# Optimization experiments

Measured on AMD Instinct MI355X. Metric: run time of the kernel, lower is better.

## Reference

```python
import jax, jax.numpy as jnp
import numpy as np
from math import sqrt

N_HEADS = 16

def setup_inputs() -> dict:
    key = jax.random.key(0)
    ks = jax.random.split(key, 6)
    B, T, C = 4, 2048, 1024
    s = 0.02
    return {
        "X": jax.random.normal(ks[0], (B, T, C), jnp.float32),
        "Wq": jax.random.normal(ks[1], (C, C), jnp.float32) * s,
        "Wk": jax.random.normal(ks[2], (C, C), jnp.float32) * s,
        "Wv": jax.random.normal(ks[3], (C, C), jnp.float32) * s,
        "Wo": jax.random.normal(ks[4], (C, C), jnp.float32) * s,
        "bo": jnp.zeros((C,), jnp.float32),
    }

def reference(X, Wq, Wk, Wv, Wo, bo):
    B, T, C = X.shape
    H = N_HEADS
    D = C // H
    scale = sqrt(C / H)  # == sqrt(D)
    # Linear layers (torch Linear: y = x @ W.T), split into heads: [B,H,T,D]
    Q = (X @ Wq.T).reshape(B, T, H, D).transpose(0, 2, 1, 3)
    K = (X @ Wk.T).reshape(B, T, H, D).transpose(0, 2, 1, 3)
    V = (X @ Wv.T).reshape(B, T, H, D).transpose(0, 2, 1, 3)
    A = jnp.einsum("bhtd,bhsd->bhts", Q, K) / scale  # [B,H,T,T]
    causal = jnp.tril(jnp.ones((T, T), dtype=bool))
    A = jnp.where(causal, A, -jnp.inf)
    A = jax.nn.softmax(A, axis=-1)
    Y = jnp.einsum("bhts,bhsd->bhtd", A, V)  # [B,H,T,D]
    Y = Y.transpose(0, 2, 1, 3).reshape(B, T, C)
    return Y @ Wo.T + bo
```

## Files before the change

### kernel.cpp

```cpp
#include <hip/hip_runtime.h>
#include <hip/hip_bf16.h>
#include <stdint.h>


typedef unsigned short u16;
typedef __attribute__((ext_vector_type(8))) __bf16 bf16x8;
typedef __attribute__((ext_vector_type(4))) float  f32x4;
typedef __attribute__((ext_vector_type(4))) unsigned short u16x4;
typedef __attribute__((ext_vector_type(8))) unsigned short u16x8;
typedef __attribute__((ext_vector_type(4))) short s16x4;

#define B_  4
#define T_  2048
#define C_  1024
#define H_  16
#define D_  64
#define BT_ (B_ * T_)
#define NT_ 16

#define Q_SCALE 0.1803368801111204f

__device__ __forceinline__ u16 f32_to_bf16(float f) {
    unsigned int u = __float_as_uint(f);
    unsigned int r = (u + 0x7FFFu + ((u >> 16) & 1u)) >> 16;
    return (u16)r;
}

__device__ __forceinline__ unsigned int pk_bf16(float a, float b) {
    float2 f2; f2.x = a; f2.y = b;
    __hip_bfloat162 h = __float22bfloat162_rn(f2);
    return *(unsigned int*)&h;
}

__device__ __forceinline__ void async16(const void* g, void* lds) {
    __builtin_amdgcn_global_load_lds(
        (const __attribute__((address_space(1))) void*)g,
        (__attribute__((address_space(3))) void*)lds, 16, 0, 0);
}

__global__ void cast_all_kernel(const float* __restrict__ X,
                                const float* __restrict__ w0, const float* __restrict__ w1,
                                const float* __restrict__ w2, const float* __restrict__ w3,
                                u16* __restrict__ xo,
                                u16* __restrict__ o0, u16* __restrict__ o1,
                                u16* __restrict__ o2, u16* __restrict__ o3) {
    int id = blockIdx.x;
    const float* in; u16* out; int i;
    if (id < 8192) {
        in = X; out = xo; i = id * 256 + threadIdx.x;
    } else {
        int k = (id - 8192) >> 10;
        in  = (k == 0) ? w0 : (k == 1) ? w1 : (k == 2) ? w2 : w3;
        out = (k == 0) ? o0 : (k == 1) ? o1 : (k == 2) ? o2 : o3;
        i = ((id - 8192) & 1023) * 256 + threadIdx.x;
    }
    float4 v = ((const float4*)in)[i];
    u16x4 o;
    o[0] = f32_to_bf16(v.x); o[1] = f32_to_bf16(v.y);
    o[2] = f32_to_bf16(v.z); o[3] = f32_to_bf16(v.w);
    ((u16x4*)out)[i] = o;
}

#define PH384(CB, P, ISSUE, GATE)                                              \
  {                                                                            \
    if ((P) == 0) {                                                            \
      _Pragma("unroll") for (int mi = 0; mi < 4; ++mi)                         \
        _Pragma("unroll") for (int ks = 0; ks < 2; ++ks)                       \
          xf[mi][ks] = *(const bf16x8*)((CB) + axoff[mi][ks]);                 \
    }                                                                          \
    _Pragma("unroll") for (int e = 0; e < 2; ++e)                              \
      _Pragma("unroll") for (int ks = 0; ks < 2; ++ks)                         \
        wf[e][ks] = *(const bf16x8*)((CB) + bwoff[2 * (P) + e][ks]);           \
    ISSUE;                                                                     \
    if ((P) == 0) asm volatile("s_waitcnt lgkmcnt(8)" ::: "memory");           \
    if ((GATE) == 6) asm volatile("s_waitcnt vmcnt(6)" ::: "memory");          \
    else if ((GATE) == 0) asm volatile("s_waitcnt vmcnt(0)" ::: "memory");     \
    __builtin_amdgcn_s_barrier();                                              \
    asm volatile("" ::: "memory");                                             \
    __builtin_amdgcn_s_setprio(1);                                             \
    _Pragma("unroll") for (int mi = 0; mi < 4; ++mi)                           \
      _Pragma("unroll") for (int e = 0; e < 2; ++e) {                          \
        f32x4 a_ = acc[mi][2 * (P) + e];                                       \
        if (SWAPV) {                                                           \
          a_ = __builtin_amdgcn_mfma_f32_16x16x32_bf16(xf[mi][0], wf[e][0], a_, 0, 0, 0); \
          a_ = __builtin_amdgcn_mfma_f32_16x16x32_bf16(xf[mi][1], wf[e][1], a_, 0, 0, 0); \
        } else {                                                               \
          a_ = __builtin_amdgcn_mfma_f32_16x16x32_bf16(wf[e][0], xf[mi][0], a_, 0, 0, 0); \
          a_ = __builtin_amdgcn_mfma_f32_16x16x32_bf16(wf[e][1], xf[mi][1], a_, 0, 0, 0); \
        }                                                                      \
        acc[mi][2 * (P) + e] = a_;                                             \
      }                                                                        \
    __builtin_amdgcn_s_setprio(0);                                             \
    asm volatile("" ::: "memory");                                             \
    __builtin_amdgcn_s_barrier();                                              \
    asm volatile("" ::: "memory");                                             \
  }

template<bool SWAPV>
__device__ __forceinline__ void qkv384_core(const u16* __restrict__ Arow,
                                            const u16* __restrict__ Brow,
                                            char* lds, f32x4 (&acc)[4][6])
{
    int tid = threadIdx.x, lane = tid & 63, w = tid >> 6;
    int quad = lane >> 4, l15 = lane & 15;
    int wm = w >> 2, wn = w & 3;

    int gc = (((tid & 7) - (tid >> 3)) & 7) * 8;
    const u16* asrc = Arow + (size_t)(tid >> 3) * C_ + gc;
    const u16* bsrc = Brow + (size_t)(tid >> 3) * C_ + gc;

    auto issue_unit = [&](int kt, int u) {
        char* d = lds + ((kt & 1) << 16) + (u << 14) + (w << 10);
        int ko = kt * 64;
        const u16* s = (u == 0) ? (asrc + ko)
                                : (bsrc + (size_t)(u - 1) * 128 * C_ + ko);
        async16(s, d);
        async16(s + (size_t)64 * C_, d + 8192);
    };

    int axoff[4][2], bwoff[6][2];
#pragma unroll
    for (int mi = 0; mi < 4; ++mi) {
        int r = wm * 64 + mi * 16 + l15;
#pragma unroll
        for (int ks = 0; ks < 2; ++ks)
            axoff[mi][ks] = r * 128 + (((ks * 4 + quad + r) & 7) << 4);
    }
#pragma unroll
    for (int nj = 0; nj < 6; ++nj) {
        int r = wn * 32 + (nj & 1) * 16 + l15;
#pragma unroll
        for (int ks = 0; ks < 2; ++ks)
            bwoff[nj][ks] = (1 + (nj >> 1)) * 16384 + r * 128 + (((ks * 4 + quad + r) & 7) << 4);
    }

    bf16x8 xf[4][2];
    bf16x8 wf[2][2];

    issue_unit(0, 0); issue_unit(0, 1); issue_unit(0, 2); issue_unit(0, 3);
    issue_unit(1, 0); issue_unit(1, 1); issue_unit(1, 2);
    asm volatile("s_waitcnt vmcnt(6)" ::: "memory");
    __builtin_amdgcn_s_barrier();
    asm volatile("" ::: "memory");

    for (int t = 0; t < NT_; ++t) {
        char* cb = lds + ((t & 1) << 16);
        PH384(cb, 0, { if (t + 1 < NT_) issue_unit(t + 1, 3); }, -1);
        PH384(cb, 1, { if (t + 2 < NT_) { issue_unit(t + 2, 0); issue_unit(t + 2, 1); } }, -1);
        int gate = (t < NT_ - 2) ? 6 : ((t == NT_ - 2) ? 0 : -1);
        PH384(cb, 2, { if (t + 2 < NT_) issue_unit(t + 2, 2); }, gate);
    }
}

__global__ __launch_bounds__(512, 2) void qkv_gemm384(
    const u16* __restrict__ Xb, const u16* __restrict__ Wcat,
    u16* __restrict__ Qb, u16* __restrict__ Kb, u16* __restrict__ Vtb)
{
    __shared__ __attribute__((aligned(128))) char LDSRAW[131072];

    int id = blockIdx.x;
    int wg = (id & 7) * 64 + (id >> 3);
    int bn = wg >> 6;
    int bm = wg & 63;
    int m0 = bm * 128;
    int chb = bn * 384;

    const u16* Arow = Xb   + (size_t)m0  * C_;
    const u16* Brow = Wcat + (size_t)chb * C_;

    f32x4 acc[4][6];
    const f32x4 z4 = {0.f, 0.f, 0.f, 0.f};
#pragma unroll
    for (int i = 0; i < 4; ++i)
#pragma unroll
        for (int j = 0; j < 6; ++j) acc[i][j] = z4;

    int tid = threadIdx.x, lane = tid & 63, w = tid >> 6;
    int quad = lane >> 4, l15 = lane & 15;
    int wm = w >> 2, wn = w & 3;

    if (bn < 6) {
        qkv384_core<false>(Arow, Brow, LDSRAW, acc);
#pragma unroll
        for (int mi = 0; mi < 4; ++mi) {
            int tg = m0 + wm * 64 + mi * 16 + l15;
#pragma unroll
            for (int nj = 0; nj < 6; ++nj) {
                int colb = chb + (nj >> 1) * 128 + wn * 32 + (nj & 1) * 16 + quad * 4;
                if (colb < 2048) {
                    u16* OUT = (colb < 1024) ? Qb : Kb;
                    float sc = (colb < 1024) ? Q_SCALE : 1.0f;
                    u16x4 v;
#pragma unroll
                    for (int rr = 0; rr < 4; ++rr) v[rr] = f32_to_bf16(acc[mi][nj][rr] * sc);
                    *(u16x4*)&OUT[(size_t)tg * C_ + (colb & 1023)] = v;
                } else {
                    int b_ = tg >> 11, tl = tg & (T_ - 1);
#pragma unroll
                    for (int rr = 0; rr < 4; ++rr) {
                        int ch = colb + rr;
                        int h = (ch >> 6) & 15, d = ch & 63;
                        Vtb[((size_t)(b_ * H_ + h) * D_ + d) * T_ + tl] =
                            f32_to_bf16(acc[mi][nj][rr]);
                    }
                }
            }
        }
    } else {
        qkv384_core<true>(Arow, Brow, LDSRAW, acc);
#pragma unroll
        for (int mi = 0; mi < 4; ++mi) {
            int t0 = m0 + wm * 64 + mi * 16 + quad * 4;
            int b_ = t0 >> 11, tl = t0 & (T_ - 1);
#pragma unroll
            for (int nj = 0; nj < 6; ++nj) {
                int ch = chb + (nj >> 1) * 128 + wn * 32 + (nj & 1) * 16 + l15;
                int h = (ch >> 6) & 15, d = ch & 63;
                u16x4 v;
#pragma unroll
                for (int rr = 0; rr < 4; ++rr) v[rr] = f32_to_bf16(acc[mi][nj][rr]);
                *(u16x4*)&Vtb[((size_t)(b_ * H_ + h) * D_ + d) * T_ + tl] = v;
            }
        }
    }
}

template<bool SWAP>
__device__ __forceinline__ void gemm8_core(const u16* __restrict__ Arow,
                                           const u16* __restrict__ Brow,
                                           char* lds, f32x4 (&acc)[4][4])
{
    int tid  = threadIdx.x;
    int lane = tid & 63, w = tid >> 6;
    int quad = lane >> 4, l15 = lane & 15;
    int wm = w >> 2, wn = w & 3;

    int r  = tid >> 2, s4 = tid & 3;
    int kg = ((s4 - (r >> 1)) & 3) * 8;
    const u16* xsrc  = Arow + (size_t)r * C_ + kg;
    const u16* wsrc0 = Brow + (size_t)r * C_ + kg;
    const u16* wsrc1 = Brow + (size_t)(128 + r) * C_ + kg;
    int wu = w << 10;

    int xoff[4], woff[4];
#pragma unroll
    for (int i = 0; i < 4; ++i) {
        int rx = wm * 64 + i * 16 + l15;
        xoff[i] = rx * 64 + (((rx >> 1) + quad) & 3) * 16;
        int rw = wn * 64 + i * 16 + l15;
        woff[i] = 16384 + rw * 64 + (((rw >> 1) + quad) & 3) * 16;
    }

    auto issue_group = [&](int g) {
        int db = (g >> 1) & 1, ks = g & 1;
        int koff = (g >> 1) * 64 + ks * 32;
        char* ldb = lds + db * 49152;
        async16(xsrc  + koff, ldb + ks * 8192 + wu);
        async16(wsrc0 + koff, ldb + 16384 + ks * 16384 + wu);
        async16(wsrc1 + koff, ldb + 16384 + ks * 16384 + 8192 + wu);
    };

    issue_group(0); issue_group(1); issue_group(2);
    asm volatile("s_waitcnt vmcnt(6)" ::: "memory");
    __builtin_amdgcn_s_barrier();
    asm volatile("" ::: "memory");

    for (int t = 0; t < NT_; ++t) {
        char* cb = lds + (t & 1) * 49152;
#pragma unroll
        for (int p = 0; p < 2; ++p) {
            bf16x8 xf[4], wf[4];
            const char* xb = cb + p * 8192;
            const char* wb = cb + p * 16384;
#pragma unroll
            for (int i = 0; i < 4; ++i) xf[i] = *(const bf16x8*)(xb + xoff[i]);
#pragma unroll
            for (int j = 0; j < 4; ++j) wf[j] = *(const bf16x8*)(wb + woff[j]);

            int g = 2 * t + 3 + p;
            if (g < 2 * NT_) issue_group(g);

            if (t < NT_ - 2) {
                asm volatile("s_waitcnt vmcnt(6)" ::: "memory");
            } else if (t == NT_ - 2) {
                if (p == 0) asm volatile("s_waitcnt vmcnt(6)" ::: "memory");
                else        asm volatile("s_waitcnt vmcnt(3)" ::: "memory");
            } else {
                if (p == 0) asm volatile("s_waitcnt vmcnt(0)" ::: "memory");
            }
            asm volatile("" ::: "memory");
            __builtin_amdgcn_s_barrier();
            asm volatile("" ::: "memory");

            __builtin_amdgcn_s_setprio(1);
#pragma unroll
            for (int i = 0; i < 4; ++i)
#pragma unroll
                for (int j = 0; j < 4; ++j) {
                    if (SWAP)
                        acc[i][j] = __builtin_amdgcn_mfma_f32_16x16x32_bf16(xf[i], wf[j], acc[i][j], 0, 0, 0);
                    else
                        acc[i][j] = __builtin_amdgcn_mfma_f32_16x16x32_bf16(wf[j], xf[i], acc[i][j], 0, 0, 0);
                }
            __builtin_amdgcn_s_setprio(0);
            asm volatile("" ::: "memory");
            __builtin_amdgcn_s_barrier();
            asm volatile("" ::: "memory");
        }
    }
}

__global__ __launch_bounds__(256, 4) void attn_kernel(
    const u16* __restrict__ Qb, const u16* __restrict__ Kb,
    const u16* __restrict__ Vtb, u16* __restrict__ Yb)
{
    __shared__ u16 SMA[16384];
    u16* Ks0 = SMA;
    u16* Ks1 = SMA + 4096;
    u16* Vs0 = SMA + 8192;
    u16* Vs1 = SMA + 12288;

    int id = blockIdx.x;
    int bh = id & 63;
    int jj = id >> 6;

    int tid = threadIdx.x, lane = tid & 63, w = tid >> 6;
    int quad = lane >> 4, l15 = lane & 15;
    int b = bh >> 4, h = bh & 15;

    int koff0[4], koff1[4], voff[4][4];
#pragma unroll
    for (int sblk = 0; sblk < 4; ++sblk) {
        int sr = sblk * 16 + l15;
        koff0[sblk] = (sr * 64 + ((quad + sr) & 7) * 8) * 2;
        koff1[sblk] = (sr * 64 + ((4 + quad + sr) & 7) * 8) * 2;
    }
#pragma unroll
    for (int n = 0; n < 4; ++n)
#pragma unroll
        for (int sblk = 0; sblk < 4; ++sblk) {
            int dr = n * 16 + l15;
            voff[n][sblk] = (dr * 64 + ((sblk * 2 + (quad >> 1) + dr) & 7) * 8 + (quad & 1) * 4) * 2;
        }

    int cA = tid, cB = tid + 256;
    int sA = cA >> 3, sB = cB >> 3;
    int offA = (((cA & 7) - sA) & 7) * 8;
    int offB = (((cB & 7) - sB) & 7) * 8;
    const u16* Kbase = Kb + (size_t)(b * T_) * C_ + h * 64;
    const u16* Vbase = Vtb + (size_t)bh * D_ * T_;
    int ldsb0 = (w * 64) * 16, ldsb1 = (256 + w * 64) * 16;

    const s16x4 ones = { (short)0x3F80, (short)0x3F80, (short)0x3F80, (short)0x3F80 };
    const f32x4 z4 = {0.f, 0.f, 0.f, 0.f};

    int qts[2] = { jj, 31 - jj };

    for (int pass = 0; pass < 2; ++pass) {
        int qt = qts[pass];
        int qbase = qt * 64;

        if (pass) __syncthreads();

        bf16x8 qf0, qf1;
        {
            const u16* q0 = Qb + ((size_t)(b * T_ + qbase + w * 16 + l15)) * C_ + h * 64;
            qf0 = *(const bf16x8*)(q0 + quad * 8);
            qf1 = *(const bf16x8*)(q0 + 32 + quad * 8);
        }

        f32x4 o_acc[4];
        f32x4 l_acc = z4;
#pragma unroll
        for (int n = 0; n < 4; ++n) o_acc[n] = z4;

        const int nst = qt + 1;

        const u16* kgpA = Kbase + (size_t)sA * C_ + offA;
        const u16* kgpB = Kbase + (size_t)sB * C_ + offB;
        const u16* vgpA = Vbase + sA * T_ + offA;
        const u16* vgpB = Vbase + sB * T_ + offB;

        async16(kgpA, (char*)Ks0 + ldsb0);
        async16(kgpB, (char*)Ks0 + ldsb1);
        async16(vgpA, (char*)Vs0 + ldsb0);
        async16(vgpB, (char*)Vs0 + ldsb1);
        kgpA += 64 * C_; kgpB += 64 * C_; vgpA += 64; vgpB += 64;

        auto tile_body = [&](int st, const u16* K_, const u16* V_, char* Kpf, char* Vpf) {
            __syncthreads();
            if (st + 1 < nst) {
                async16(kgpA, Kpf + ldsb0);
                async16(kgpB, Kpf + ldsb1);
                async16(vgpA, Vpf + ldsb0);
                async16(vgpB, Vpf + ldsb1);
            }
            kgpA += 64 * C_; kgpB += 64 * C_; vgpA += 64; vgpB += 64;

            f32x4 sv[4];
#pragma unroll
            for (int sblk = 0; sblk < 4; ++sblk) {
                bf16x8 k0 = *(const bf16x8*)((const char*)K_ + koff0[sblk]);
                bf16x8 k1 = *(const bf16x8*)((const char*)K_ + koff1[sblk]);
                f32x4 t0 = __builtin_amdgcn_mfma_f32_16x16x32_bf16(k0, qf0, z4, 0, 0, 0);
                sv[sblk] = __builtin_amdgcn_mfma_f32_16x16x32_bf16(k1, qf1, t0, 0, 0, 0);
            }

            if (st == qt) {
                int tl = w * 16 + l15;
#pragma unroll
                for (int sblk = 0; sblk < 4; ++sblk)
#pragma unroll
                    for (int r = 0; r < 4; ++r)
                        if (sblk * 16 + quad * 4 + r > tl) sv[sblk][r] = -1e30f;
            }

            s16x4 pfrag[4];
#pragma unroll
            for (int sblk = 0; sblk < 4; ++sblk) {
#pragma unroll
                for (int r = 0; r < 4; ++r)
                    sv[sblk][r] = __builtin_amdgcn_exp2f(sv[sblk][r]);
                uint2 pk;
                pk.x = pk_bf16(sv[sblk][0], sv[sblk][1]);
                pk.y = pk_bf16(sv[sblk][2], sv[sblk][3]);
                pfrag[sblk] = *(s16x4*)&pk;
                l_acc = __builtin_amdgcn_mfma_f32_16x16x16bf16_1k(ones, pfrag[sblk], l_acc, 0, 0, 0);
            }

#pragma unroll
            for (int n = 0; n < 4; ++n)
#pragma unroll
                for (int sblk = 0; sblk < 4; ++sblk) {
                    s16x4 va = *(const s16x4*)((const char*)V_ + voff[n][sblk]);
                    o_acc[n] = __builtin_amdgcn_mfma_f32_16x16x16bf16_1k(va, pfrag[sblk], o_acc[n], 0, 0, 0);
                }
        };

        for (int st = 0; st < nst; st += 2) {
            tile_body(st, Ks0, Vs0, (char*)Ks1, (char*)Vs1);
            if (st + 1 < nst)
                tile_body(st + 1, Ks1, Vs1, (char*)Ks0, (char*)Vs0);
        }

        __syncthreads();
        u16* PW = SMA + w * 1152;
        {
            float inv = 1.0f / l_acc[0];
#pragma unroll
            for (int n = 0; n < 4; ++n) {
                uint2 pk;
                pk.x = pk_bf16(o_acc[n][0] * inv, o_acc[n][1] * inv);
                pk.y = pk_bf16(o_acc[n][2] * inv, o_acc[n][3] * inv);
                *(u16x4*)&PW[l15 * 72 + n * 16 + quad * 4] = *(u16x4*)&pk;
            }
        }
        asm volatile("s_waitcnt lgkmcnt(0)" ::: "memory");
#pragma unroll
        for (int st = 0; st < 2; ++st) {
            int tr = st * 8 + (lane >> 3);
            int d8 = (lane & 7) * 8;
            u16x8 v = *(u16x8*)&PW[tr * 72 + d8];
            *(u16x8*)&Yb[(size_t)(b * T_ + qbase + w * 16 + tr) * C_ + h * 64 + d8] = v;
        }
    }
}

__global__ __launch_bounds__(512, 2) void proj_gemm8(
    const u16* __restrict__ Yb, const u16* __restrict__ Wob,
    const float* __restrict__ bo, float* __restrict__ out)
{
    __shared__ __attribute__((aligned(128))) char LDSRAW[98304];

    int id = blockIdx.x;
    int wg = (id & 7) * 32 + (id >> 3);
    int bm = wg >> 2, bn = wg & 3;
    int m0 = bm * 128, n0 = bn * 256;

    f32x4 acc[4][4];
    const f32x4 z4 = {0.f, 0.f, 0.f, 0.f};
#pragma unroll
    for (int i = 0; i < 4; ++i)
#pragma unroll
        for (int j = 0; j < 4; ++j) acc[i][j] = z4;

    gemm8_core<false>(Yb + (size_t)m0 * C_, Wob + (size_t)n0 * C_, LDSRAW, acc);

    int tid = threadIdx.x, lane = tid & 63, w = tid >> 6;
    int quad = lane >> 4, l15 = lane & 15;
    int wm = w >> 2, wn = w & 3;

#pragma unroll
    for (int j = 0; j < 4; ++j) {
        int ch = n0 + wn * 64 + j * 16 + quad * 4;
        f32x4 bv = *(const f32x4*)&bo[ch];
#pragma unroll
        for (int i = 0; i < 4; ++i) {
            int t = m0 + wm * 64 + i * 16 + l15;
            f32x4 v = acc[i][j] + bv;
            *(f32x4*)&out[(size_t)t * C_ + ch] = v;
        }
    }
}

extern "C" void kernel_launch(void* const* d_in, const int* in_sizes, int n_in,
                              void* d_out, int out_size, void* d_ws, size_t ws_size,
                              hipStream_t stream) {
    const float* X  = (const float*)d_in[0];
    const float* Wq = (const float*)d_in[1];
    const float* Wk = (const float*)d_in[2];
    const float* Wv = (const float*)d_in[3];
    const float* Wo = (const float*)d_in[4];
    const float* bo = (const float*)d_in[5];

    char* ws = (char*)d_ws;
    u16* Xb  = (u16*)(ws);
    u16* Wqb = (u16*)(ws + (16u << 20));
    u16* Wkb = (u16*)(ws + (18u << 20));
    u16* Wvb = (u16*)(ws + (20u << 20));
    u16* Wob = (u16*)(ws + (22u << 20));
    u16* Qb  = (u16*)(ws + (24u << 20));
    u16* Kb  = (u16*)(ws + (40u << 20));
    u16* Vtb = (u16*)(ws + (56u << 20));
    u16* Yb  = (u16*)(ws + (72u << 20));

    cast_all_kernel<<<dim3(8192 + 4 * 1024), 256, 0, stream>>>(
        X, Wq, Wk, Wv, Wo, Xb, Wqb, Wkb, Wvb, Wob);

    qkv_gemm384<<<dim3(512), 512, 0, stream>>>(Xb, Wqb, Qb, Kb, Vtb);
    attn_kernel<<<dim3(1024), 256, 0, stream>>>(Qb, Kb, Vtb, Yb);
    proj_gemm8<<<dim3(256), 512, 0, stream>>>(Yb, Wob, bo, (float*)d_out);
}
```

Baseline: 228.4 us.

## Double-buffer LDS fragment reads across phases in QKV and projection GEMMs

Both GEMM cores now prefetch the next phase's LDS fragments into a second register set, issuing the reads after the barrier and before the MFMA block, which is fenced with sched_barrier. In the old code each phase loaded its own fragments and then waited on them, so LDS latency was exposed before every MFMA burst. The QKV loop is unrolled by two to ping-pong the register sets, and the projection GEMM gets a matching ping-pong restructure. This raises register pressure and relies on the waitcnt and barrier placement staying correct for the LDS buffer reuse.

```diff
diff --git a/kernel.cpp b/kernel.cpp
--- a/kernel.cpp
+++ b/kernel.cpp
@@ -61,40 +61,51 @@
     ((u16x4*)out)[i] = o;
 }
 
-#define PH384(CB, P, ISSUE, GATE)                                              \
-  {                                                                            \
-    if ((P) == 0) {                                                            \
-      _Pragma("unroll") for (int mi = 0; mi < 4; ++mi)                         \
-        _Pragma("unroll") for (int ks = 0; ks < 2; ++ks)                       \
-          xf[mi][ks] = *(const bf16x8*)((CB) + axoff[mi][ks]);                 \
-    }                                                                          \
-    _Pragma("unroll") for (int e = 0; e < 2; ++e)                              \
-      _Pragma("unroll") for (int ks = 0; ks < 2; ++ks)                         \
-        wf[e][ks] = *(const bf16x8*)((CB) + bwoff[2 * (P) + e][ks]);           \
-    ISSUE;                                                                     \
-    if ((P) == 0) asm volatile("s_waitcnt lgkmcnt(8)" ::: "memory");           \
-    if ((GATE) == 6) asm volatile("s_waitcnt vmcnt(6)" ::: "memory");          \
-    else if ((GATE) == 0) asm volatile("s_waitcnt vmcnt(0)" ::: "memory");     \
-    __builtin_amdgcn_s_barrier();                                              \
-    asm volatile("" ::: "memory");                                             \
-    __builtin_amdgcn_s_setprio(1);                                             \
-    _Pragma("unroll") for (int mi = 0; mi < 4; ++mi)                           \
-      _Pragma("unroll") for (int e = 0; e < 2; ++e) {                          \
-        f32x4 a_ = acc[mi][2 * (P) + e];                                       \
-        if (SWAPV) {                                                           \
-          a_ = __builtin_amdgcn_mfma_f32_16x16x32_bf16(xf[mi][0], wf[e][0], a_, 0, 0, 0); \
-          a_ = __builtin_amdgcn_mfma_f32_16x16x32_bf16(xf[mi][1], wf[e][1], a_, 0, 0, 0); \
-        } else {                                                               \
-          a_ = __builtin_amdgcn_mfma_f32_16x16x32_bf16(wf[e][0], xf[mi][0], a_, 0, 0, 0); \
-          a_ = __builtin_amdgcn_mfma_f32_16x16x32_bf16(wf[e][1], xf[mi][1], a_, 0, 0, 0); \
-        }                                                                      \
-        acc[mi][2 * (P) + e] = a_;                                             \
-      }                                                                        \
-    __builtin_amdgcn_s_setprio(0);                                             \
-    asm volatile("" ::: "memory");                                             \
-    __builtin_amdgcn_s_barrier();                                              \
-    asm volatile("" ::: "memory");                                             \
+#define RD_WF(CB, P, DST)                                                        \
+    _Pragma("unroll") for (int e_ = 0; e_ < 2; ++e_)                             \
+      _Pragma("unroll") for (int ks_ = 0; ks_ < 2; ++ks_)                        \
+        DST[e_][ks_] = *(const bf16x8*)((CB) + bwoff[2 * (P) + e_][ks_]);
+
+#define RD_XF(CB, DST)                                                           \
+    _Pragma("unroll") for (int mi_ = 0; mi_ < 4; ++mi_)                          \
+      _Pragma("unroll") for (int ks_ = 0; ks_ < 2; ++ks_)                        \
+        DST[mi_][ks_] = *(const bf16x8*)((CB) + axoff[mi_][ks_]);
+
+#define PH3(ISSUE, GATE, XF, WF, PIDX, ...)                                      \
+  {                                                                              \
+    ISSUE;                                                                       \
+    if ((GATE) == 6)      asm volatile("s_waitcnt vmcnt(6)" ::: "memory");       \
+    else if ((GATE) == 0) asm volatile("s_waitcnt vmcnt(0)" ::: "memory");       \
+    __builtin_amdgcn_s_barrier();                                                \
+    asm volatile("" ::: "memory");                                               \
+    __VA_ARGS__;                                                                 \
+    __builtin_amdgcn_sched_barrier(0);                                           \
+    __builtin_amdgcn_s_setprio(1);                                               \
+    _Pragma("unroll") for (int mi = 0; mi < 4; ++mi)                             \
+      _Pragma("unroll") for (int e = 0; e < 2; ++e) {                            \
+        f32x4 a_ = acc[mi][2 * (PIDX) + e];                                      \
+        if (SWAPV) {                                                             \
+          a_ = __builtin_amdgcn_mfma_f32_16x16x32_bf16(XF[mi][0], WF[e][0], a_, 0, 0, 0); \
+          a_ = __builtin_amdgcn_mfma_f32_16x16x32_bf16(XF[mi][1], WF[e][1], a_, 0, 0, 0); \
+        } else {                                                                 \
+          a_ = __builtin_amdgcn_mfma_f32_16x16x32_bf16(WF[e][0], XF[mi][0], a_, 0, 0, 0); \
+          a_ = __builtin_amdgcn_mfma_f32_16x16x32_bf16(WF[e][1], XF[mi][1], a_, 0, 0, 0); \
+        }                                                                        \
+        acc[mi][2 * (PIDX) + e] = a_;                                            \
+      }                                                                          \
+    __builtin_amdgcn_s_setprio(0);                                               \
+    asm volatile("" ::: "memory");                                               \
+    __builtin_amdgcn_s_barrier();                                                \
+    asm volatile("" ::: "memory");                                               \
   }
+
+#define TILE3(T, CB, CBN, XFC, XFN, WF0, WF1, GU3, GNX, GATE_P2, RDN)            \
+  PH3({ if (GU3) issue_unit((T) + 1, 3); }, -1, XFC, WF0, 0,                     \
+      { RD_WF(CB, 1, WF1); });                                                   \
+  PH3({ if (GNX) { issue_unit((T) + 2, 0); issue_unit((T) + 2, 1); } }, -1,      \
+      XFC, WF1, 1, { RD_WF(CB, 2, WF0); });                                      \
+  PH3({ if (GNX) issue_unit((T) + 2, 2); }, GATE_P2, XFC, WF0, 2,                \
+      { if (RDN) { RD_XF(CBN, XFN); RD_WF(CBN, 0, WF1); } });
 
 template<bool SWAPV>
 __device__ __forceinline__ void qkv384_core(const u16* __restrict__ Arow,
@@ -134,22 +145,26 @@
             bwoff[nj][ks] = (1 + (nj >> 1)) * 16384 + r * 128 + (((ks * 4 + quad + r) & 7) << 4);
     }
 
-    bf16x8 xf[4][2];
-    bf16x8 wf[2][2];
+    bf16x8 xfA[4][2], xfB[4][2];
+    bf16x8 wfA[2][2], wfB[2][2];
+
+    char* db0 = lds;
+    char* db1 = lds + 65536;
 
     issue_unit(0, 0); issue_unit(0, 1); issue_unit(0, 2); issue_unit(0, 3);
     issue_unit(1, 0); issue_unit(1, 1); issue_unit(1, 2);
     asm volatile("s_waitcnt vmcnt(6)" ::: "memory");
     __builtin_amdgcn_s_barrier();
     asm volatile("" ::: "memory");
-
-    for (int t = 0; t < NT_; ++t) {
-        char* cb = lds + ((t & 1) << 16);
-        PH384(cb, 0, { if (t + 1 < NT_) issue_unit(t + 1, 3); }, -1);
-        PH384(cb, 1, { if (t + 2 < NT_) { issue_unit(t + 2, 0); issue_unit(t + 2, 1); } }, -1);
-        int gate = (t < NT_ - 2) ? 6 : ((t == NT_ - 2) ? 0 : -1);
-        PH384(cb, 2, { if (t + 2 < NT_) issue_unit(t + 2, 2); }, gate);
-    }
+    RD_XF(db0, xfA);
+    RD_WF(db0, 0, wfA);
+
+    for (int t = 0; t < NT_ - 2; t += 2) {
+        TILE3(t,     db0, db1, xfA, xfB, wfA, wfB, 1, 1, 6, 1);
+        TILE3(t + 1, db1, db0, xfB, xfA, wfB, wfA, 1, 1, 6, 1);
+    }
+    TILE3(NT_ - 2, db0, db1, xfA, xfB, wfA, wfB, 1, 0, 0, 1);
+    TILE3(NT_ - 1, db1, db0, xfB, xfA, wfB, wfA, 0, 0, -1, 0);
 }
 
 __global__ __launch_bounds__(512, 2) void qkv_gemm384(
@@ -225,10 +240,35 @@
     }
 }
 
-template<bool SWAP>
-__device__ __forceinline__ void gemm8_core(const u16* __restrict__ Arow,
-                                           const u16* __restrict__ Brow,
-                                           char* lds, f32x4 (&acc)[4][4])
+#define RD8(CB, KS, FX, FW)                                                      \
+    _Pragma("unroll") for (int i_ = 0; i_ < 4; ++i_) {                           \
+        FX[i_] = *(const bf16x8*)((CB) + (KS) * 8192  + xoff[i_]);               \
+        FW[i_] = *(const bf16x8*)((CB) + (KS) * 16384 + woff[i_]);               \
+    }
+
+#define PPH(ISSUE, GATE, FX, FW, ...)                                            \
+  {                                                                              \
+    ISSUE;                                                                       \
+    if ((GATE) == 6)      asm volatile("s_waitcnt vmcnt(6)" ::: "memory");       \
+    else if ((GATE) == 3) asm volatile("s_waitcnt vmcnt(3)" ::: "memory");       \
+    else if ((GATE) == 0) asm volatile("s_waitcnt vmcnt(0)" ::: "memory");       \
+    __builtin_amdgcn_s_barrier();                                                \
+    asm volatile("" ::: "memory");                                               \
+    __VA_ARGS__;                                                                 \
+    __builtin_amdgcn_sched_barrier(0);                                           \
+    __builtin_amdgcn_s_setprio(1);                                               \
+    _Pragma("unroll") for (int i = 0; i < 4; ++i)                                \
+      _Pragma("unroll") for (int j = 0; j < 4; ++j)                              \
+        acc[i][j] = __builtin_amdgcn_mfma_f32_16x16x32_bf16(FW[j], FX[i], acc[i][j], 0, 0, 0); \
+    __builtin_amdgcn_s_setprio(0);                                               \
+    asm volatile("" ::: "memory");                                               \
+    __builtin_amdgcn_s_barrier();                                                \
+    asm volatile("" ::: "memory");                                               \
+  }
+
+__device__ __forceinline__ void gemm8p_core(const u16* __restrict__ Arow,
+                                            const u16* __restrict__ Brow,
+                                            char* lds, f32x4 (&acc)[4][4])
 {
     int tid  = threadIdx.x;
     int lane = tid & 63, w = tid >> 6;
@@ -260,53 +300,28 @@
         async16(wsrc1 + koff, ldb + 16384 + ks * 16384 + 8192 + wu);
     };
 
+    bf16x8 fAx[4], fAw[4], fBx[4], fBw[4];
+
     issue_group(0); issue_group(1); issue_group(2);
     asm volatile("s_waitcnt vmcnt(6)" ::: "memory");
     __builtin_amdgcn_s_barrier();
     asm volatile("" ::: "memory");
-
-    for (int t = 0; t < NT_; ++t) {
-        char* cb = lds + (t & 1) * 49152;
-#pragma unroll
-        for (int p = 0; p < 2; ++p) {
-            bf16x8 xf[4], wf[4];
-            const char* xb = cb + p * 8192;
-            const char* wb = cb + p * 16384;
-#pragma unroll
-            for (int i = 0; i < 4; ++i) xf[i] = *(const bf16x8*)(xb + xoff[i]);
-#pragma unroll
-            for (int j = 0; j < 4; ++j) wf[j] = *(const bf16x8*)(wb + woff[j]);
-
-            int g = 2 * t + 3 + p;
-            if (g < 2 * NT_) issue_group(g);
-
-            if (t < NT_ - 2) {
-                asm volatile("s_waitcnt vmcnt(6)" ::: "memory");
-            } else if (t == NT_ - 2) {
-                if (p == 0) asm volatile("s_waitcnt vmcnt(6)" ::: "memory");
-                else        asm volatile("s_waitcnt vmcnt(3)" ::: "memory");
-            } else {
-                if (p == 0) asm volatile("s_waitcnt vmcnt(0)" ::: "memory");
-            }
-            asm volatile("" ::: "memory");
-            __builtin_amdgcn_s_barrier();
-            asm volatile("" ::: "memory");
-
-            __builtin_amdgcn_s_setprio(1);
-#pragma unroll
-            for (int i = 0; i < 4; ++i)
-#pragma unroll
-                for (int j = 0; j < 4; ++j) {
-                    if (SWAP)
-                        acc[i][j] = __builtin_amdgcn_mfma_f32_16x16x32_bf16(xf[i], wf[j], acc[i][j], 0, 0, 0);
-                    else
-                        acc[i][j] = __builtin_amdgcn_mfma_f32_16x16x32_bf16(wf[j], xf[i], acc[i][j], 0, 0, 0);
-                }
-            __builtin_amdgcn_s_setprio(0);
-            asm volatile("" ::: "memory");
-            __builtin_amdgcn_s_barrier();
-            asm volatile("" ::: "memory");
-        }
+    RD8(lds, 0, fAx, fAw);
+
+    for (int t = 0; t < NT_ - 1; ++t) {
+        char* cb  = lds + (t & 1) * 49152;
+        char* cbn = lds + ((t + 1) & 1) * 49152;
+        PPH({ issue_group(2 * t + 3); }, 6, fAx, fAw, { RD8(cb, 1, fBx, fBw); });
+        if (t < NT_ - 2) {
+            PPH({ issue_group(2 * t + 4); }, 6, fBx, fBw, { RD8(cbn, 0, fAx, fAw); });
+        } else {
+            PPH({}, 3, fBx, fBw, { RD8(cbn, 0, fAx, fAw); });
+        }
+    }
+    {
+        char* cb = lds + ((NT_ - 1) & 1) * 49152;
+        PPH({}, 0, fAx, fAw, { RD8(cb, 1, fBx, fBw); });
+        PPH({}, -1, fBx, fBw, {});
     }
 }
 
@@ -484,7 +499,7 @@
 #pragma unroll
         for (int j = 0; j < 4; ++j) acc[i][j] = z4;
 
-    gemm8_core<false>(Yb + (size_t)m0 * C_, Wob + (size_t)n0 * C_, LDSRAW, acc);
+    gemm8p_core(Yb + (size_t)m0 * C_, Wob + (size_t)n0 * C_, LDSRAW, acc);
 
     int tid = threadIdx.x, lane = tid & 63, w = tid >> 6;
     int quad = lane >> 4, l15 = lane & 15;
```

After: 229.9 us. No clear change (+0.6%).
